# Optimization experiments

Measured on AMD Instinct MI355X. Metric: run time of the kernel, lower is better.

Reference implementation:

```python
import jax, jax.numpy as jnp
import numpy as np

IN_FEATURES = 512
OUT_FEATURES = 512
GRID_MIN = -2.0
GRID_MAX = 2.0
NUM_GRIDS = 8
SPLINE_SCALE = 0.1
BATCH = 16384


def setup_inputs() -> dict:
    key = jax.random.key(0)
    kx, kw = jax.random.split(key)
    x = jax.random.normal(kx, (BATCH, IN_FEATURES), dtype=jnp.float32)
    grid = jnp.linspace(GRID_MIN, GRID_MAX, NUM_GRIDS, dtype=jnp.float32)
    spline_weight = (
        jax.random.normal(kw, (IN_FEATURES * NUM_GRIDS, OUT_FEATURES), dtype=jnp.float32)
        * SPLINE_SCALE
    )
    return {"x": x, "grid": grid, "spline_weight": spline_weight}


def reference(x, grid, spline_weight):
    # denominator h = (grid_max - grid_min) / (num_grids - 1)
    h = (GRID_MAX - GRID_MIN) / (NUM_GRIDS - 1)
    # basis: [B, in_features, num_grids]
    basis = jnp.exp(-jnp.square((x[..., None] - grid) / h))
    # flatten to [B, in_features * num_grids] and GEMM
    return basis.reshape(basis.shape[0], -1) @ spline_weight
```

## Files before the change

kernel.cpp:

```cpp
#include <hip/hip_runtime.h>
#include <hip/hip_bf16.h>

#define BATCH 16384
#define IN_F 512
#define OUT_F 512
#define NG 8
#define KTOT (IN_F * NG)

#define SH    2.1019642153762872f
#define SSTEP 1.2011224087864498f
#define BC0N  4.2039284307525745f
#define RC1   2.4022448175728996f

typedef __attribute__((ext_vector_type(8))) short short8;
typedef __attribute__((ext_vector_type(4))) float f32x4;
typedef __attribute__((ext_vector_type(2))) float f32x2;
typedef __attribute__((ext_vector_type(4))) unsigned int u32x4;
typedef __attribute__((ext_vector_type(2))) unsigned int u32x2;

__device__ __forceinline__ unsigned fbits(float f) {
    union { float f; unsigned u; } v; v.f = f; return v.u;
}
__device__ __forceinline__ unsigned pack2bf(float lo, float hi) {
    return __builtin_amdgcn_perm(fbits(hi) + 0x8000u, fbits(lo) + 0x8000u,
                                 0x07060302u);
}

__device__ __forceinline__ void lds_barrier() {
    __asm__ volatile("" ::: "memory");
    __builtin_amdgcn_sched_barrier(0);
    __builtin_amdgcn_s_waitcnt(0xC07F);
    __builtin_amdgcn_s_barrier();
    __builtin_amdgcn_sched_barrier(0);
    __asm__ volatile("" ::: "memory");
}

__global__ void wt_swizzle(const float* __restrict__ W, unsigned short* __restrict__ Wt) {
    const int gid  = blockIdx.x * 256 + threadIdx.x;
    const int lane = gid & 63;
    const int f    = (gid >> 6) & 7;
    const int kt   = (gid >> 9) & 63;
    const int s    = gid >> 15;
    const int j  = f & 3, kk = f >> 2;
    const int l15 = lane & 15, lq = lane >> 4;
    const int n  = s * 64 + j * 16 + l15;
    const int k0 = kt * 64 + kk * 32 + lq * 8;
    constexpr float QS[8] = {1.0f,
                             3.6787944117144233e-1f,
                             1.8315638888734179e-2f,
                             1.2340980408667956e-4f,
                             1.1253517471925912e-7f,
                             1.3887943864964021e-11f,
                             2.3195228302435693e-16f,
                             5.2428856633634640e-22f};
    u32x4 pk;
#pragma unroll
    for (int e = 0; e < 4; ++e)
        pk[e] = pack2bf(W[(size_t)(k0 + 2 * e) * OUT_F + n] * QS[2 * e],
                        W[(size_t)(k0 + 2 * e + 1) * OUT_F + n] * QS[2 * e + 1]);
    *(u32x4*)(Wt + (size_t)gid * 8) = pk;
}

__global__ __launch_bounds__(256, 2) void gauss_gemm9(
        const float* __restrict__ X, const unsigned short* __restrict__ Wt,
        float* __restrict__ Out) {
    __shared__ __align__(16) unsigned short sA[2 * 64 * 64];

    const int tid  = threadIdx.x;
    const int lane = tid & 63;
    const int wave = tid >> 6;
    const int nb = (blockIdx.x & 7) * 64 + (blockIdx.x >> 3);
    const int cb = nb >> 8;
    const int rb = nb & 255;
    const int m0 = rb * 64;
    const int n0 = cb * 256;
    const int l15 = lane & 15;
    const int lq  = lane >> 4;
    const int s   = cb * 4 + wave;

    const int aw0 = lane * 64 + (((2 * wave)     ^ (lane & 7)) << 3);
    const int aw1 = lane * 64 + (((2 * wave + 1) ^ (lane & 7)) << 3);
    const float* xlp = X + (size_t)(m0 + lane) * IN_F + wave * 2;

    int aofs[2][4];
#pragma unroll
    for (int kk = 0; kk < 2; ++kk)
#pragma unroll
        for (int i = 0; i < 4; ++i)
            aofs[kk][i] = (i * 16 + l15) * 64 + (((kk * 4 + lq) ^ (l15 & 7)) << 3);

    const unsigned short* bptr = Wt + (size_t)s * 262144 + lane * 8;

    f32x4 acc[4][4];
#pragma unroll
    for (int i = 0; i < 4; ++i)
#pragma unroll
        for (int j = 0; j < 4; ++j)
            acc[i][j] = (f32x4){0.f, 0.f, 0.f, 0.f};

    auto stageA = [&](f32x2 xv, int buf) {
        unsigned short* base = sA + buf * 4096;
#pragma unroll
        for (int h = 0; h < 2; ++h) {
            const float t0  = fmaf(h ? xv.y : xv.x, SH, BC0N);
            const float rho = __builtin_amdgcn_exp2f(t0 * RC1);
            const float v0  = __builtin_amdgcn_exp2f(-t0 * t0);
            const float v1 = v0 * rho;
            const float v2 = v1 * rho;
            const float v3 = v2 * rho;
            const float v4 = v3 * rho;
            const float v5 = v4 * rho;
            const float v6 = v5 * rho;
            const float v7 = v6 * rho;
            u32x4 pk;
            pk[0] = pack2bf(v0, v1);
            pk[1] = pack2bf(v2, v3);
            pk[2] = pack2bf(v4, v5);
            pk[3] = pack2bf(v6, v7);
            *(u32x4*)(base + (h ? aw1 : aw0)) = pk;
        }
    };

    short8 bfA[8], bfB[8];
    f32x2 xr;

    {
        f32x2 x0 = *(const f32x2*)(xlp);
        stageA(x0, 0);
#pragma unroll
        for (int f = 0; f < 8; ++f)
            bfA[f] = *(const short8*)(bptr + f * 512);
        xr = *(const f32x2*)(xlp + 8);
        lds_barrier();
    }

#define GG_ITER(KT, BUF, BU, BF)                                               \
    {                                                                          \
        const int kn1 = ((KT) + 1 < 63) ? (KT) + 1 : 63;                       \
        const int kn2 = ((KT) + 2 < 63) ? (KT) + 2 : 63;                       \
        _Pragma("unroll")                                                      \
        for (int f = 0; f < 8; ++f)                                            \
            BF[f] = *(const short8*)(bptr + (size_t)kn1 * 4096 + f * 512);     \
        short8 af[2][4];                                                       \
        _Pragma("unroll")                                                      \
        for (int kk = 0; kk < 2; ++kk)                                         \
            _Pragma("unroll")                                                  \
            for (int i = 0; i < 4; ++i)                                        \
                af[kk][i] = *(const short8*)(sA + (BUF) * 4096 + aofs[kk][i]); \
        f32x2 xn = *(const f32x2*)(xlp + (size_t)kn2 * 8);                     \
        stageA(xr, (BUF) ^ 1);                                                 \
        xr = xn;                                                               \
        __builtin_amdgcn_s_setprio(1);                                         \
        _Pragma("unroll")                                                      \
        for (int kk = 0; kk < 2; ++kk)                                         \
            _Pragma("unroll")                                                  \
            for (int i = 0; i < 4; ++i)                                        \
                _Pragma("unroll")                                              \
                for (int j = 0; j < 4; ++j)                                    \
                    acc[i][j] = __builtin_amdgcn_mfma_f32_16x16x32_bf16(       \
                        af[kk][i], BU[kk * 4 + j], acc[i][j], 0, 0, 0);        \
        __builtin_amdgcn_s_setprio(0);                                         \
        lds_barrier();                                                         \
    }

    for (int kt = 0; kt < 64; kt += 2) {
        GG_ITER(kt,     0, bfA, bfB)
        GG_ITER(kt + 1, 1, bfB, bfA)
    }
#undef GG_ITER

#pragma unroll
    for (int i = 0; i < 4; ++i) {
        const int r0 = m0 + i * 16 + lq * 4;
#pragma unroll
        for (int j = 0; j < 4; ++j) {
            const int c = n0 + wave * 64 + j * 16 + l15;
#pragma unroll
            for (int e = 0; e < 4; ++e)
                Out[(size_t)(r0 + e) * OUT_F + c] = acc[i][j][e];
        }
    }
}

#define BM 128
#define BN 128
#define BK 64
#define LDA 72
#define LDB 72

__global__ __launch_bounds__(256, 2) void gauss_gemm_fb(
        const float* __restrict__ X, const float* __restrict__ W,
        float* __restrict__ Out) {
    __shared__ __align__(16) unsigned short sA[BM * LDA];
    __shared__ __align__(16) unsigned short sB2[BN * LDB];

    const int tid  = threadIdx.x;
    const int lane = tid & 63;
    const int wave = tid >> 6;
    const int rb = blockIdx.x >> 2;
    const int cbx = blockIdx.x & 3;
    const int m0 = rb * BM;
    const int n0 = cbx * BN;
    const int wr = (wave >> 1) * 64;
    const int wc = (wave & 1) * 64;
    const int l15 = lane & 15;
    const int lq  = lane >> 4;

    f32x4 acc[4][4];
#pragma unroll
    for (int i = 0; i < 4; ++i)
#pragma unroll
        for (int j = 0; j < 4; ++j)
            acc[i][j] = (f32x4){0.f, 0.f, 0.f, 0.f};

    const int arow = tid & 127;
    const int axq  = tid >> 7;

    for (int kt = 0; kt < KTOT / BK; ++kt) {
        const int k0  = kt * BK;
        const int xc0 = kt * (BK / NG);

        const f32x4 xv = *(const f32x4*)(X + (size_t)(m0 + arow) * IN_F + xc0 + 4 * axq);
        unsigned short* sArow = sA + arow * LDA + axq * 32;
#pragma unroll
        for (int j = 0; j < 4; ++j) {
            const float xs = xv[j] * SH;
            u32x4 pk;
#pragma unroll
            for (int g = 0; g < 8; g += 2) {
                float t0 = xs + (BC0N - g * SSTEP);
                float t1 = xs + (BC0N - (g + 1) * SSTEP);
                pk[g >> 1] = pack2bf(__builtin_amdgcn_exp2f(-t0 * t0),
                                     __builtin_amdgcn_exp2f(-t1 * t1));
            }
            *(u32x4*)(sArow + j * 8) = pk;
        }

#pragma unroll
        for (int p = 0; p < 8; ++p) {
            int id = p * 256 + tid;
            int n  = id & 127;
            int k4 = id >> 7;
            const float* wp = W + (size_t)(k0 + k4 * 4) * OUT_F + n0 + n;
            u32x2 v;
            v[0] = pack2bf(wp[0], wp[OUT_F]);
            v[1] = pack2bf(wp[2 * OUT_F], wp[3 * OUT_F]);
            *(u32x2*)(sB2 + n * LDB + k4 * 4) = v;
        }

        __syncthreads();

#pragma unroll
        for (int kk = 0; kk < BK; kk += 32) {
            short8 af[4], bfv[4];
#pragma unroll
            for (int i = 0; i < 4; ++i)
                af[i] = *(const short8*)(sA + (wr + i * 16 + l15) * LDA + kk + lq * 8);
#pragma unroll
            for (int i = 0; i < 4; ++i)
                bfv[i] = *(const short8*)(sB2 + (wc + i * 16 + l15) * LDB + kk + lq * 8);
#pragma unroll
            for (int i = 0; i < 4; ++i)
#pragma unroll
                for (int j = 0; j < 4; ++j)
                    acc[i][j] = __builtin_amdgcn_mfma_f32_16x16x32_bf16(af[i], bfv[j], acc[i][j], 0, 0, 0);
        }

        __syncthreads();
    }

#pragma unroll
    for (int i = 0; i < 4; ++i) {
        const int r0 = m0 + wr + i * 16 + lq * 4;
#pragma unroll
        for (int j = 0; j < 4; ++j) {
            const int c = n0 + wc + j * 16 + l15;
#pragma unroll
            for (int e = 0; e < 4; ++e)
                Out[(size_t)(r0 + e) * OUT_F + c] = acc[i][j][e];
        }
    }
}

extern "C" void kernel_launch(void* const* d_in, const int* in_sizes, int n_in,
                              void* d_out, int out_size, void* d_ws, size_t ws_size,
                              hipStream_t stream) {
    (void)in_sizes; (void)n_in; (void)out_size;
    const float* X = (const float*)d_in[0];
    const float* W = (const float*)d_in[2];
    float* Out = (float*)d_out;

    const size_t wt_bytes = (size_t)KTOT * OUT_F * sizeof(unsigned short);
    if (ws_size >= wt_bytes) {
        unsigned short* Wt = (unsigned short*)d_ws;
        wt_swizzle<<<dim3(KTOT * OUT_F / 8 / 256), 256, 0, stream>>>(W, Wt);
        gauss_gemm9<<<dim3((BATCH / 64) * (OUT_F / 256)), 256, 0, stream>>>(X, Wt, Out);
    } else {
        gauss_gemm_fb<<<dim3((BATCH / BM) * (OUT_F / BN)), 256, 0, stream>>>(X, W, Out);
    }
}
```

Baseline: 150.9 us.

## Pre-swizzle X into MFMA fragment layout and compute basis in registers, dropping LDS

Adds a prep kernel that transposes X into a per-lane fragment order alongside the weight swizzle. The new GEMM kernel then loads X directly into registers, computes the Gaussian basis fragments per lane and feeds them to the MFMAs. This removes LDS staging and the per-iteration block barriers. The cost is an extra full pass over X (32 MB read and write) and redundant basis computation across the four waves, since each wave recomputes the same A fragments.

```diff
diff --git a/kernel.cpp b/kernel.cpp
--- a/kernel.cpp
+++ b/kernel.cpp
@@ -24,6 +24,26 @@
 __device__ __forceinline__ unsigned pack2bf(float lo, float hi) {
     return __builtin_amdgcn_perm(fbits(hi) + 0x8000u, fbits(lo) + 0x8000u,
                                  0x07060302u);
+}
+
+__device__ __forceinline__ short8 basis_frag(float x) {
+    const float t0  = fmaf(x, SH, BC0N);
+    const float rho = __builtin_amdgcn_exp2f(t0 * RC1);
+    const float v0  = __builtin_amdgcn_exp2f(-t0 * t0);
+    const float v1 = v0 * rho;
+    const float v2 = v1 * rho;
+    const float v3 = v2 * rho;
+    const float v4 = v3 * rho;
+    const float v5 = v4 * rho;
+    const float v6 = v5 * rho;
+    const float v7 = v6 * rho;
+    u32x4 pk;
+    pk[0] = pack2bf(v0, v1);
+    pk[1] = pack2bf(v2, v3);
+    pk[2] = pack2bf(v4, v5);
+    pk[3] = pack2bf(v6, v7);
+    union { u32x4 u; short8 s; } cv; cv.u = pk;
+    return cv.s;
 }
 
 __device__ __forceinline__ void lds_barrier() {
@@ -33,6 +53,135 @@
     __builtin_amdgcn_s_barrier();
     __builtin_amdgcn_sched_barrier(0);
     __asm__ volatile("" ::: "memory");
+}
+
+__global__ void prep_all(const float* __restrict__ W, const float* __restrict__ X,
+                         unsigned short* __restrict__ Wt, float* __restrict__ XtF) {
+    const int tid = threadIdx.x;
+    if (blockIdx.x < 1024) {
+        const int gid  = blockIdx.x * 256 + tid;
+        const int lane = gid & 63;
+        const int f    = (gid >> 6) & 7;
+        const int kt   = (gid >> 9) & 63;
+        const int s    = gid >> 15;
+        const int j  = f & 3, kk = f >> 2;
+        const int l15 = lane & 15, lq = lane >> 4;
+        const int n  = s * 64 + j * 16 + l15;
+        const int k0 = kt * 64 + kk * 32 + lq * 8;
+        constexpr float QS[8] = {1.0f,
+                                 3.6787944117144233e-1f,
+                                 1.8315638888734179e-2f,
+                                 1.2340980408667956e-4f,
+                                 1.1253517471925912e-7f,
+                                 1.3887943864964021e-11f,
+                                 2.3195228302435693e-16f,
+                                 5.2428856633634640e-22f};
+        u32x4 pk;
+#pragma unroll
+        for (int e = 0; e < 4; ++e)
+            pk[e] = pack2bf(W[(size_t)(k0 + 2 * e) * OUT_F + n] * QS[2 * e],
+                            W[(size_t)(k0 + 2 * e + 1) * OUT_F + n] * QS[2 * e + 1]);
+        *(u32x4*)(Wt + (size_t)gid * 8) = pk;
+    } else {
+        const int bid2 = blockIdx.x - 1024;
+        const int rb   = bid2 >> 4;
+        const int ktq  = bid2 & 15;
+        const int ktl  = tid >> 6;
+        const int lane = tid & 63;
+        const int kt   = ktq * 4 + ktl;
+        const int l15 = lane & 15, lq = lane >> 4;
+        float v[8];
+#pragma unroll
+        for (int e = 0; e < 8; ++e) {
+            const int i  = e & 3, kk = e >> 2;
+            const int m  = rb * 64 + i * 16 + l15;
+            const int c  = kt * 8 + kk * 4 + lq;
+            v[e] = X[(size_t)m * IN_F + c];
+        }
+        float* dst = XtF + ((size_t)(rb * 64 + kt) * 64 + lane) * 8;
+        *(f32x4*)(dst)     = (f32x4){v[0], v[1], v[2], v[3]};
+        *(f32x4*)(dst + 4) = (f32x4){v[4], v[5], v[6], v[7]};
+    }
+}
+
+__global__ __launch_bounds__(256, 2) void gauss_gemm10(
+        const float* __restrict__ XtF, const unsigned short* __restrict__ Wt,
+        float* __restrict__ Out) {
+    const int tid  = threadIdx.x;
+    const int lane = tid & 63;
+    const int wave = tid >> 6;
+    const int nb = (blockIdx.x & 7) * 64 + (blockIdx.x >> 3);
+    const int cb = nb >> 8;
+    const int rb = nb & 255;
+    const int m0 = rb * 64;
+    const int n0 = cb * 256;
+    const int l15 = lane & 15;
+    const int lq  = lane >> 4;
+    const int s   = cb * 4 + wave;
+
+    const unsigned short* bptr = Wt + (size_t)s * 262144 + lane * 8;
+    const float* aptr = XtF + (size_t)rb * 32768 + (size_t)lane * 8;
+
+    f32x4 acc[4][4];
+#pragma unroll
+    for (int i = 0; i < 4; ++i)
+#pragma unroll
+        for (int j = 0; j < 4; ++j)
+            acc[i][j] = (f32x4){0.f, 0.f, 0.f, 0.f};
+
+    short8 bfA[8], bfB[8];
+    f32x4 xaA0, xaA1, xaB0, xaB1;
+
+    xaA0 = *(const f32x4*)(aptr);
+    xaA1 = *(const f32x4*)(aptr + 4);
+#pragma unroll
+    for (int f = 0; f < 8; ++f)
+        bfA[f] = *(const short8*)(bptr + f * 512);
+
+#define GG_ITER(KT, BU, BF, XU0, XU1, XF0, XF1)                                \
+    {                                                                          \
+        const int kn1 = ((KT) + 1 < 63) ? (KT) + 1 : 63;                       \
+        XF0 = *(const f32x4*)(aptr + kn1 * 512);                               \
+        XF1 = *(const f32x4*)(aptr + kn1 * 512 + 4);                           \
+        _Pragma("unroll")                                                      \
+        for (int f = 0; f < 8; ++f)                                            \
+            BF[f] = *(const short8*)(bptr + (size_t)kn1 * 4096 + f * 512);     \
+        short8 af[2][4];                                                       \
+        _Pragma("unroll")                                                      \
+        for (int i = 0; i < 4; ++i)                                            \
+            af[0][i] = basis_frag(XU0[i]);                                     \
+        _Pragma("unroll")                                                      \
+        for (int i = 0; i < 4; ++i)                                            \
+            af[1][i] = basis_frag(XU1[i]);                                     \
+        __builtin_amdgcn_s_setprio(1);                                         \
+        _Pragma("unroll")                                                      \
+        for (int kk = 0; kk < 2; ++kk)                                         \
+            _Pragma("unroll")                                                  \
+            for (int i = 0; i < 4; ++i)                                        \
+                _Pragma("unroll")                                              \
+                for (int j = 0; j < 4; ++j)                                    \
+                    acc[i][j] = __builtin_amdgcn_mfma_f32_16x16x32_bf16(       \
+                        af[kk][i], BU[kk * 4 + j], acc[i][j], 0, 0, 0);        \
+        __builtin_amdgcn_s_setprio(0);                                         \
+    }
+
+    for (int kt = 0; kt < 64; kt += 2) {
+        GG_ITER(kt,     bfA, bfB, xaA0, xaA1, xaB0, xaB1)
+        GG_ITER(kt + 1, bfB, bfA, xaB0, xaB1, xaA0, xaA1)
+    }
+#undef GG_ITER
+
+#pragma unroll
+    for (int i = 0; i < 4; ++i) {
+        const int r0 = m0 + i * 16 + lq * 4;
+#pragma unroll
+        for (int j = 0; j < 4; ++j) {
+            const int c = n0 + wave * 64 + j * 16 + l15;
+#pragma unroll
+            for (int e = 0; e < 4; ++e)
+                Out[(size_t)(r0 + e) * OUT_F + c] = acc[i][j][e];
+        }
+    }
 }
 
 __global__ void wt_swizzle(const float* __restrict__ W, unsigned short* __restrict__ Wt) {
@@ -134,7 +283,7 @@
         lds_barrier();
     }
 
-#define GG_ITER(KT, BUF, BU, BF)                                               \
+#define GG_ITER9(KT, BUF, BU, BF)                                              \
     {                                                                          \
         const int kn1 = ((KT) + 1 < 63) ? (KT) + 1 : 63;                       \
         const int kn2 = ((KT) + 2 < 63) ? (KT) + 2 : 63;                       \
@@ -164,10 +313,10 @@
     }
 
     for (int kt = 0; kt < 64; kt += 2) {
-        GG_ITER(kt,     0, bfA, bfB)
-        GG_ITER(kt + 1, 1, bfB, bfA)
-    }
-#undef GG_ITER
+        GG_ITER9(kt,     0, bfA, bfB)
+        GG_ITER9(kt + 1, 1, bfB, bfA)
+    }
+#undef GG_ITER9
 
 #pragma unroll
     for (int i = 0; i < 4; ++i) {
@@ -290,8 +439,14 @@
     const float* W = (const float*)d_in[2];
     float* Out = (float*)d_out;
 
-    const size_t wt_bytes = (size_t)KTOT * OUT_F * sizeof(unsigned short);
-    if (ws_size >= wt_bytes) {
+    const size_t wt_bytes  = (size_t)KTOT * OUT_F * sizeof(unsigned short);
+    const size_t xtf_bytes = (size_t)BATCH * IN_F * sizeof(float);
+    if (ws_size >= wt_bytes + xtf_bytes) {
+        unsigned short* Wt = (unsigned short*)d_ws;
+        float* XtF = (float*)((char*)d_ws + wt_bytes);
+        prep_all<<<dim3(1024 + 4096), 256, 0, stream>>>(W, X, Wt, XtF);
+        gauss_gemm10<<<dim3((BATCH / 64) * (OUT_F / 256)), 256, 0, stream>>>(XtF, Wt, Out);
+    } else if (ws_size >= wt_bytes) {
         unsigned short* Wt = (unsigned short*)d_ws;
         wt_swizzle<<<dim3(KTOT * OUT_F / 8 / 256), 256, 0, stream>>>(W, Wt);
         gauss_gemm9<<<dim3((BATCH / 64) * (OUT_F / 256)), 256, 0, stream>>>(X, Wt, Out);
```

Result: slower. 182.8 us (+21.2%).

## Use 8-slot LDS ring to barrier every four k-tiles; use hardware bf16 pack

Applied to the files above, without the earlier changes.

The A-operand LDS buffer grows from 2 to 8 slots, so the Gaussian basis is staged four k-tiles ahead and the workgroup barrier runs once per four iterations instead of every iteration. X loads are prefetched further ahead, alternating between two registers. The bf16 packing switches from perm-based rounding to the v_cvt_pk_bf16_f32 instruction. LDS use rises from 16KB to 64KB per block, which could limit occupancy at two blocks per CU.

```diff
diff --git a/kernel.cpp b/kernel.cpp
--- a/kernel.cpp
+++ b/kernel.cpp
@@ -24,6 +24,11 @@
 __device__ __forceinline__ unsigned pack2bf(float lo, float hi) {
     return __builtin_amdgcn_perm(fbits(hi) + 0x8000u, fbits(lo) + 0x8000u,
                                  0x07060302u);
+}
+__device__ __forceinline__ unsigned cvtpk(float lo, float hi) {
+    unsigned r;
+    asm("v_cvt_pk_bf16_f32 %0, %1, %2" : "=v"(r) : "v"(lo), "v"(hi));
+    return r;
 }
 
 __device__ __forceinline__ void lds_barrier() {
@@ -61,10 +66,10 @@
     *(u32x4*)(Wt + (size_t)gid * 8) = pk;
 }
 
-__global__ __launch_bounds__(256, 2) void gauss_gemm9(
+__global__ __launch_bounds__(256, 2) void gauss_gemm12(
         const float* __restrict__ X, const unsigned short* __restrict__ Wt,
         float* __restrict__ Out) {
-    __shared__ __align__(16) unsigned short sA[2 * 64 * 64];
+    __shared__ __align__(16) unsigned short sA[8 * 4096];
 
     const int tid  = threadIdx.x;
     const int lane = tid & 63;
@@ -98,8 +103,8 @@
         for (int j = 0; j < 4; ++j)
             acc[i][j] = (f32x4){0.f, 0.f, 0.f, 0.f};
 
-    auto stageA = [&](f32x2 xv, int buf) {
-        unsigned short* base = sA + buf * 4096;
+    auto stageA = [&](f32x2 xv, int slot) {
+        unsigned short* base = sA + slot * 4096;
 #pragma unroll
         for (int h = 0; h < 2; ++h) {
             const float t0  = fmaf(h ? xv.y : xv.x, SH, BC0N);
@@ -113,31 +118,39 @@
             const float v6 = v5 * rho;
             const float v7 = v6 * rho;
             u32x4 pk;
-            pk[0] = pack2bf(v0, v1);
-            pk[1] = pack2bf(v2, v3);
-            pk[2] = pack2bf(v4, v5);
-            pk[3] = pack2bf(v6, v7);
+            pk[0] = cvtpk(v0, v1);
+            pk[1] = cvtpk(v2, v3);
+            pk[2] = cvtpk(v4, v5);
+            pk[3] = cvtpk(v6, v7);
             *(u32x4*)(base + (h ? aw1 : aw0)) = pk;
         }
     };
 
     short8 bfA[8], bfB[8];
-    f32x2 xr;
+    f32x2 xu, xv;
 
     {
         f32x2 x0 = *(const f32x2*)(xlp);
-        stageA(x0, 0);
+        f32x2 x1 = *(const f32x2*)(xlp + 8);
+        f32x2 x2 = *(const f32x2*)(xlp + 16);
+        f32x2 x3 = *(const f32x2*)(xlp + 24);
+        xu = *(const f32x2*)(xlp + 32);
+        xv = *(const f32x2*)(xlp + 40);
 #pragma unroll
         for (int f = 0; f < 8; ++f)
             bfA[f] = *(const short8*)(bptr + f * 512);
-        xr = *(const f32x2*)(xlp + 8);
+        stageA(x0, 0);
+        stageA(x1, 1);
+        stageA(x2, 2);
+        stageA(x3, 3);
         lds_barrier();
     }
 
-#define GG_ITER(KT, BUF, BU, BF)                                               \
+#define GG12(KT0, S, BU, BF, XUSE)                                             \
     {                                                                          \
-        const int kn1 = ((KT) + 1 < 63) ? (KT) + 1 : 63;                       \
-        const int kn2 = ((KT) + 2 < 63) ? (KT) + 2 : 63;                       \
+        const int kt  = (KT0) + (S);                                           \
+        const int kn1 = (kt + 1 < 64) ? kt + 1 : 63;                           \
+        const int kn6 = (kt + 6 < 64) ? kt + 6 : 63;                           \
         _Pragma("unroll")                                                      \
         for (int f = 0; f < 8; ++f)                                            \
             BF[f] = *(const short8*)(bptr + (size_t)kn1 * 4096 + f * 512);     \
@@ -146,10 +159,9 @@
         for (int kk = 0; kk < 2; ++kk)                                         \
             _Pragma("unroll")                                                  \
             for (int i = 0; i < 4; ++i)                                        \
-                af[kk][i] = *(const short8*)(sA + (BUF) * 4096 + aofs[kk][i]); \
-        f32x2 xn = *(const f32x2*)(xlp + (size_t)kn2 * 8);                     \
-        stageA(xr, (BUF) ^ 1);                                                 \
-        xr = xn;                                                               \
+                af[kk][i] = *(const short8*)(sA + (S) * 4096 + aofs[kk][i]);   \
+        stageA(XUSE, ((S) + 4) & 7);                                           \
+        XUSE = *(const f32x2*)(xlp + (size_t)kn6 * 8);                         \
         __builtin_amdgcn_s_setprio(1);                                         \
         _Pragma("unroll")                                                      \
         for (int kk = 0; kk < 2; ++kk)                                         \
@@ -160,14 +172,20 @@
                     acc[i][j] = __builtin_amdgcn_mfma_f32_16x16x32_bf16(       \
                         af[kk][i], BU[kk * 4 + j], acc[i][j], 0, 0, 0);        \
         __builtin_amdgcn_s_setprio(0);                                         \
-        lds_barrier();                                                         \
-    }
-
-    for (int kt = 0; kt < 64; kt += 2) {
-        GG_ITER(kt,     0, bfA, bfB)
-        GG_ITER(kt + 1, 1, bfB, bfA)
-    }
-#undef GG_ITER
+        if (((S) & 3) == 3) lds_barrier();                                     \
+    }
+
+    for (int kt0 = 0; kt0 < 64; kt0 += 8) {
+        GG12(kt0, 0, bfA, bfB, xu)
+        GG12(kt0, 1, bfB, bfA, xv)
+        GG12(kt0, 2, bfA, bfB, xu)
+        GG12(kt0, 3, bfB, bfA, xv)
+        GG12(kt0, 4, bfA, bfB, xu)
+        GG12(kt0, 5, bfB, bfA, xv)
+        GG12(kt0, 6, bfA, bfB, xu)
+        GG12(kt0, 7, bfB, bfA, xv)
+    }
+#undef GG12
 
 #pragma unroll
     for (int i = 0; i < 4; ++i) {
@@ -294,7 +312,7 @@
     if (ws_size >= wt_bytes) {
         unsigned short* Wt = (unsigned short*)d_ws;
         wt_swizzle<<<dim3(KTOT * OUT_F / 8 / 256), 256, 0, stream>>>(W, Wt);
-        gauss_gemm9<<<dim3((BATCH / 64) * (OUT_F / 256)), 256, 0, stream>>>(X, Wt, Out);
+        gauss_gemm12<<<dim3((BATCH / 64) * (OUT_F / 256)), 256, 0, stream>>>(X, Wt, Out);
     } else {
         gauss_gemm_fb<<<dim3((BATCH / BM) * (OUT_F / BN)), 256, 0, stream>>>(X, W, Out);
     }
```

New measurement: 149.3 us. No clear change (-1.0%).
